# Performance work log

Hardware: AMD Instinct MI355X
Metric: run time of the kernel (lower is better)

Reference implementation:

```python
import jax, jax.numpy as jnp
import numpy as np

HEADS = 16
DIM_HEAD = 64
LN_EPS = 1e-5
COS_EPS = 1e-8


def setup_inputs() -> dict:
    key = jax.random.key(0)
    ks = jax.random.split(key, 5)
    dim = 1024
    inner = HEADS * DIM_HEAD
    q = jax.random.normal(ks[0], (4, 1024, dim), dtype=jnp.float32)
    k = jax.random.normal(ks[1], (4, 2048, dim), dtype=jnp.float32)
    v = jax.random.normal(ks[2], (4, 2048, dim), dtype=jnp.float32)
    W_in = jax.random.normal(ks[3], (dim, inner), dtype=jnp.float32) * (1.0 / np.sqrt(dim))
    W_out = jax.random.normal(ks[4], (inner, dim), dtype=jnp.float32) * (1.0 / np.sqrt(inner))
    ln_gamma = jnp.ones((dim,), dtype=jnp.float32)
    ln_beta = jnp.zeros((dim,), dtype=jnp.float32)
    b_out = jnp.zeros((dim,), dtype=jnp.float32)
    return {"q": q, "k": k, "v": v, "ln_gamma": ln_gamma, "ln_beta": ln_beta,
            "W_in": W_in, "W_out": W_out, "b_out": b_out}


def _layernorm(x, gamma, beta):
    mu = jnp.mean(x, axis=-1, keepdims=True)
    var = jnp.mean(jnp.square(x - mu), axis=-1, keepdims=True)  # biased, as torch
    return (x - mu) * jax.lax.rsqrt(var + LN_EPS) * gamma + beta


def _project(t, gamma, beta, W_in):
    # LayerNorm -> Linear(no bias) -> split heads: b n (h d) -> b h n d
    x = _layernorm(t, gamma, beta) @ W_in
    b, n, _ = x.shape
    return x.reshape(b, n, HEADS, DIM_HEAD).transpose(0, 2, 1, 3)


def reference(q, k, v, ln_gamma, ln_beta, W_in, W_out, b_out):
    f_q = _project(q, ln_gamma, ln_beta, W_in)  # [b,h,n,d]
    f_k = _project(k, ln_gamma, ln_beta, W_in)  # [b,h,m,d]
    f_v = _project(v, ln_gamma, ln_beta, W_in)  # [b,h,m,d]
    dots = jnp.einsum('bhnd,bhmd->bhnm', f_q, f_k)
    qn = jnp.linalg.norm(f_q, axis=-1, keepdims=True)          # [b,h,n,1]
    kn = jnp.linalg.norm(f_k, axis=-1, keepdims=True)          # [b,h,m,1]
    attn = dots / (qn * kn.transpose(0, 1, 3, 2) + COS_EPS)    # [b,h,n,m]
    out = jnp.einsum('bhnm,bhmd->bhnd', attn, f_v)             # [b,h,n,d]
    b, h, n, d = out.shape
    out = out.transpose(0, 2, 1, 3).reshape(b, n, h * d)       # b n (h d)
    return out @ W_out + b_out
```

## Files before the change

### kernel.cpp

```cpp
#include <hip/hip_runtime.h>

constexpr int BATCH = 4;
constexpr int SEQQ  = 1024;
constexpr int SEQK  = 2048;
constexpr int DIM   = 1024;
constexpr int NH    = 16;
constexpr int DH    = 64;
constexpr int RQ    = BATCH * SEQQ;
constexpr int RK    = BATCH * SEQK;
constexpr int RTOT  = RQ + 2 * RK;
constexpr int BH    = BATCH * NH;
constexpr int NSLC  = 8;
constexpr float LN_EPS = 1e-5f;

typedef _Float16 f16;
typedef __attribute__((ext_vector_type(8))) _Float16 f16x8;
typedef __attribute__((ext_vector_type(4))) float f32x4;

__device__ __forceinline__ void async16(const void* g, void* l) {
  __builtin_amdgcn_global_load_lds(
      (const __attribute__((address_space(1))) void*)g,
      (__attribute__((address_space(3))) void*)l, 16, 0, 0);
}

__global__ void __launch_bounds__(256) pre_kernel(
    const float* __restrict__ q, const float* __restrict__ k,
    const float* __restrict__ v, const float* __restrict__ gamma,
    const float* __restrict__ beta, f16* __restrict__ a_h,
    const float* __restrict__ W0, const float* __restrict__ W1,
    f16* __restrict__ T0, f16* __restrict__ T1) {
  __shared__ float tile[32][33];
  if (blockIdx.x < RTOT / 4) {
    const int row = blockIdx.x * 4 + (threadIdx.x >> 6);
    const int lane = threadIdx.x & 63;
    const float* src;
    if (row < RQ)            src = q + (size_t)row * DIM;
    else if (row < RQ + RK)  src = k + (size_t)(row - RQ) * DIM;
    else                     src = v + (size_t)(row - RQ - RK) * DIM;
    float4 x[4];
    float s = 0.f, s2 = 0.f;
#pragma unroll
    for (int c = 0; c < 4; c++) {
      x[c] = ((const float4*)src)[c * 64 + lane];
      s  += x[c].x + x[c].y + x[c].z + x[c].w;
      s2 += x[c].x * x[c].x + x[c].y * x[c].y + x[c].z * x[c].z + x[c].w * x[c].w;
    }
#pragma unroll
    for (int off = 1; off < 64; off <<= 1) {
      s  += __shfl_xor(s, off);
      s2 += __shfl_xor(s2, off);
    }
    const float mu = s / DIM;
    const float rs = rsqrtf(s2 / DIM - mu * mu + LN_EPS);
#pragma unroll
    for (int c = 0; c < 4; c++) {
      float4 g = ((const float4*)gamma)[c * 64 + lane];
      float4 b = ((const float4*)beta)[c * 64 + lane];
      union { f16 h[4]; uint2 u; } o;
      o.h[0] = (f16)((x[c].x - mu) * rs * g.x + b.x);
      o.h[1] = (f16)((x[c].y - mu) * rs * g.y + b.y);
      o.h[2] = (f16)((x[c].z - mu) * rs * g.z + b.z);
      o.h[3] = (f16)((x[c].w - mu) * rs * g.w + b.w);
      ((uint2*)(a_h + (size_t)row * DIM))[c * 64 + lane] = o.u;
    }
  } else {
    const int tz = blockIdx.x - RTOT / 4;
    const float* W = (tz >= 1024) ? W1 : W0;
    f16* T = (tz >= 1024) ? T1 : T0;
    const int rem = tz & 1023;
    const int k0 = (rem & 31) * 32, n0 = (rem >> 5) * 32;
    int tx = threadIdx.x & 31, ty = threadIdx.x >> 5;
#pragma unroll
    for (int i = 0; i < 4; i++)
      tile[ty + 8 * i][tx] = W[(size_t)(k0 + ty + 8 * i) * DIM + n0 + tx];
    __syncthreads();
#pragma unroll
    for (int i = 0; i < 4; i++)
      T[(size_t)(n0 + ty + 8 * i) * DIM + k0 + tx] = (f16)tile[tx][ty + 8 * i];
  }
}

constexpr int PT_A = 320 * 64;
constexpr int PT_B = 256 * 64;

#define STAGE_A(buf, kt) do {                                        \
    const f16* s_ = gA + (size_t)(kt) * 64;                          \
    f16* d_ = AsW + (buf) * PT_A;                                    \
    async16(s_,          d_);                                        \
    async16(s_ +  65536, d_ + 4096);                                 \
    async16(s_ + 131072, d_ + 8192);                                 \
    async16(s_ + 196608, d_ + 12288);                                \
    async16(s_ + 262144, d_ + 16384);                                \
  } while (0)

#define STAGE_B(buf, kt) do {                                        \
    const f16* s_ = gB + (size_t)(kt) * 64;                          \
    f16* d_ = BsW + (buf) * PT_B;                                    \
    async16(s_,          d_);                                        \
    async16(s_ +  65536, d_ + 4096);                                 \
    async16(s_ + 131072, d_ + 8192);                                 \
    async16(s_ + 196608, d_ + 12288);                                \
  } while (0)

#define STAGE_AB(buf, kt) do { STAGE_A(buf, kt); STAGE_B(buf, kt); } while (0)

#define WT0 asm volatile("s_waitcnt vmcnt(0)" ::: "memory")
#define WTN ((void)0)
#define STN ((void)0)

#define HALF(BUF, H)                                                 \
    _Pragma("unroll") for (int j_ = 0; j_ < 4; ++j_)                 \
      bf[j_] = *(const f16x8*)(bB##H + (BUF) * PT_B + j_ * 1024);    \
    _Pragma("unroll") for (int f_ = 0; f_ < 5; ++f_)                 \
      af0[f_] = *(const f16x8*)(aB##H + (BUF) * PT_A + f_ * 1024);   \
    _Pragma("unroll") for (int f_ = 0; f_ < 5; ++f_)                 \
      af1[f_] = *(const f16x8*)(aB##H + (BUF) * PT_A + 5120 +        \
                                f_ * 1024);                          \
    __builtin_amdgcn_s_setprio(1);                                   \
    _Pragma("unroll") for (int f_ = 0; f_ < 5; ++f_)                 \
      _Pragma("unroll") for (int j_ = 0; j_ < 4; ++j_)               \
        acc[f_][j_] = __builtin_amdgcn_mfma_f32_16x16x32_f16(        \
            af0[f_], bf[j_], acc[f_][j_], 0, 0, 0);                  \
    _Pragma("unroll") for (int f_ = 0; f_ < 5; ++f_)                 \
      _Pragma("unroll") for (int j_ = 0; j_ < 4; ++j_)               \
        acc[5 + f_][j_] = __builtin_amdgcn_mfma_f32_16x16x32_f16(    \
            af1[f_], bf[j_], acc[5 + f_][j_], 0, 0, 0);              \
    __builtin_amdgcn_s_setprio(0);

#define PTILE(BUF, STG, TVW) {                                       \
    __builtin_amdgcn_s_barrier();                                    \
    __builtin_amdgcn_sched_barrier(0);                               \
    STG;                                                             \
    HALF(BUF, 0)                                                     \
    HALF(BUF, 1)                                                     \
    __builtin_amdgcn_sched_barrier(0);                               \
    TVW;                                                             \
  }

__global__ void __launch_bounds__(512, 2) proj_gemm(
    const f16* __restrict__ A, const f16* __restrict__ Bt,
    f16* __restrict__ C) {
  __shared__ __align__(16) f16 As[2 * PT_A];
  __shared__ __align__(16) f16 Bs[2 * PT_B];

  const int tid = threadIdx.x;
  const int wid = tid >> 6;
  const int lane = tid & 63;
  const int la15 = lane & 15;

  const int bid = blockIdx.x;
  const int swz = (bid & 7) * 32 + (bid >> 3);
  const int row0 = (swz >> 2) * 320;
  const int col0 = (swz & 3) * 256;

  const int wm = (wid >> 2) * 160;
  const int wn = (wid & 3) * 64;

  const int hs = (tid & 7) ^ ((tid >> 3) & 7);
  const f16* gA = A + (size_t)(row0 + (tid >> 3)) * DIM + (hs >> 2) * 32 +
                  (hs & 3) * 8;
  const f16* gB = Bt + (size_t)(col0 + (tid >> 3)) * DIM + (hs >> 2) * 32 +
                  (hs & 3) * 8;
  f16* AsW = As + wid * 512;
  f16* BsW = Bs + wid * 512;

  const int g = lane >> 4;
  const int r7 = la15 & 7;
  const int cs0 = (g ^ r7) * 8;
  const int cs1 = ((4 + g) ^ r7) * 8;
  const f16* aB0 = As + (wm + la15) * 64 + cs0;
  const f16* aB1 = As + (wm + la15) * 64 + cs1;
  const f16* bB0 = Bs + (wn + la15) * 64 + cs0;
  const f16* bB1 = Bs + (wn + la15) * 64 + cs1;

  f32x4 acc[10][4];
#pragma unroll
  for (int i = 0; i < 10; i++)
#pragma unroll
    for (int j = 0; j < 4; j++) acc[i][j] = (f32x4){0.f, 0.f, 0.f, 0.f};
  f16x8 af0[5], af1[5], bf[4];

  STAGE_AB(0, 0);
  __builtin_amdgcn_sched_barrier(0);
  WT0;

#pragma unroll 1
  for (int it = 0; it < 7; ++it) {
    const int t1 = 2 * it + 1, t2 = 2 * it + 2;
    PTILE(0, STAGE_AB(1, t1), WT0)
    PTILE(1, STAGE_AB(0, t2), WT0)
  }
  PTILE(0, STAGE_AB(1, 15), WT0)
  PTILE(1, STN, WTN)

  const int crow = (lane >> 4) * 4;
#pragma unroll
  for (int mh = 0; mh < 2; ++mh)
#pragma unroll
    for (int f = 0; f < 5; ++f) {
      const int m = mh * 5 + f;
      const int rbase = row0 + wm + mh * 80 + f * 16 + crow;
#pragma unroll
      for (int r = 0; r < 4; ++r) {
        float s = acc[m][0][r] * acc[m][0][r] + acc[m][1][r] * acc[m][1][r]
                + acc[m][2][r] * acc[m][2][r] + acc[m][3][r] * acc[m][3][r];
        s += __shfl_xor(s, 1);
        s += __shfl_xor(s, 2);
        s += __shfl_xor(s, 4);
        s += __shfl_xor(s, 8);
        if (rbase + r < RQ + RK) {
          const float inv = rsqrtf(s);
#pragma unroll
          for (int j = 0; j < 4; ++j) acc[m][j][r] *= inv;
        }
      }
    }

  f16* sc = As;
  const int wmi = wid >> 2;
  const int ehalf = tid >> 8;
  const int err = (tid >> 4) & 15;
  const int ecc = tid & 15;
  const f16* rb_l = sc + ehalf * (16 * 264) + err * 264 + ecc * 16;
#pragma unroll
  for (int mh = 0; mh < 2; ++mh)
#pragma unroll
    for (int f = 0; f < 5; ++f) {
      const int m = mh * 5 + f;
#pragma unroll
      for (int j = 0; j < 4; ++j)
#pragma unroll
        for (int r = 0; r < 4; ++r)
          sc[wmi * (16 * 264) + (crow + r) * 264 + wn + j * 16 + la15] =
              (f16)acc[m][j][r];
      __syncthreads();
      f16x8 v0 = *(const f16x8*)(rb_l);
      f16x8 v1 = *(const f16x8*)(rb_l + 8);
      const int grow = row0 + ehalf * 160 + mh * 80 + f * 16 + err;
      f16* Cp = C + (size_t)grow * DIM + col0 + ecc * 16;
      *(f16x8*)(Cp) = v0;
      *(f16x8*)(Cp + 8) = v1;
      if (!(mh == 1 && f == 4)) __syncthreads();
    }
}

__global__ void __launch_bounds__(256) s_kernel(
    const f16* __restrict__ f, float* __restrict__ S4) {
  const int bh = blockIdx.x;
  const int b = bh >> 4, h = bh & 15;
  const int mbase = blockIdx.y * (SEQK / NSLC);
  const int t = threadIdx.x;
  __shared__ float ks[32][68];
  __shared__ float vs[32][68];
  const int lm   = t >> 3;
  const int lseg = (t & 7) * 8;
  const int d1 = (t & 15) * 4;
  const int d2 = (t >> 4) * 4;
  float acc[4][4] = {{0.f}};
  const f16* fk_base = f + ((size_t)RQ + (size_t)b * SEQK) * DIM + h * DH;
  const f16* fv_base = f + ((size_t)RQ + RK + (size_t)b * SEQK) * DIM + h * DH;

  int m = mbase + lm;
  f16x8 kv = *(const f16x8*)(fk_base + (size_t)m * DIM + lseg);
  f16x8 vv = *(const f16x8*)(fv_base + (size_t)m * DIM + lseg);

  constexpr int SUBS = SEQK / NSLC / 32;
  for (int sub = 0; sub < SUBS; ++sub) {
    __syncthreads();
#pragma unroll
    for (int e = 0; e < 8; e++) {
      ks[lm][lseg + e] = (float)kv[e];
      vs[lm][lseg + e] = (float)vv[e];
    }
    __syncthreads();
    if (sub + 1 < SUBS) {
      m = mbase + (sub + 1) * 32 + lm;
      kv = *(const f16x8*)(fk_base + (size_t)m * DIM + lseg);
      vv = *(const f16x8*)(fv_base + (size_t)m * DIM + lseg);
    }
#pragma unroll
    for (int mm = 0; mm < 32; ++mm) {
      float4 kk = *(const float4*)&ks[mm][d1];
      float4 vv2 = *(const float4*)&vs[mm][d2];
      acc[0][0] = fmaf(kk.x, vv2.x, acc[0][0]);
      acc[0][1] = fmaf(kk.x, vv2.y, acc[0][1]);
      acc[0][2] = fmaf(kk.x, vv2.z, acc[0][2]);
      acc[0][3] = fmaf(kk.x, vv2.w, acc[0][3]);
      acc[1][0] = fmaf(kk.y, vv2.x, acc[1][0]);
      acc[1][1] = fmaf(kk.y, vv2.y, acc[1][1]);
      acc[1][2] = fmaf(kk.y, vv2.z, acc[1][2]);
      acc[1][3] = fmaf(kk.y, vv2.w, acc[1][3]);
      acc[2][0] = fmaf(kk.z, vv2.x, acc[2][0]);
      acc[2][1] = fmaf(kk.z, vv2.y, acc[2][1]);
      acc[2][2] = fmaf(kk.z, vv2.z, acc[2][2]);
      acc[2][3] = fmaf(kk.z, vv2.w, acc[2][3]);
      acc[3][0] = fmaf(kk.w, vv2.x, acc[3][0]);
      acc[3][1] = fmaf(kk.w, vv2.y, acc[3][1]);
      acc[3][2] = fmaf(kk.w, vv2.z, acc[3][2]);
      acc[3][3] = fmaf(kk.w, vv2.w, acc[3][3]);
    }
  }
  float* Sp = S4 + ((size_t)blockIdx.y * BH + bh) * DH * DH;
#pragma unroll
  for (int i = 0; i < 4; i++)
#pragma unroll
    for (int j = 0; j < 4; j++)
      Sp[(d1 + i) * DH + (d2 + j)] = acc[i][j];
}

__global__ void __launch_bounds__(256) s_reduce(
    const float* __restrict__ S4, f16* __restrict__ Sh) {
  const int bh = blockIdx.x;
  const int t = threadIdx.x;
  const size_t base = (size_t)bh * DH * DH + t * 16;
  constexpr size_t STR = (size_t)BH * DH * DH;
#pragma unroll
  for (int c = 0; c < 4; c++) {
    float4 s = {0.f, 0.f, 0.f, 0.f};
#pragma unroll
    for (int p = 0; p < NSLC; p++) {
      float4 sp = *(const float4*)(S4 + base + p * STR + 4 * c);
      s.x += sp.x; s.y += sp.y; s.z += sp.z; s.w += sp.w;
    }
    union { f16 h[4]; uint2 u; } o;
    o.h[0] = (f16)s.x; o.h[1] = (f16)s.y; o.h[2] = (f16)s.z; o.h[3] = (f16)s.w;
    *(uint2*)(Sh + base + 4 * c) = o.u;
  }
}

__global__ void __launch_bounds__(256) m_build(
    const f16* __restrict__ wt_out, const f16* __restrict__ Sh,
    f16* __restrict__ Mt) {
  const int n0 = blockIdx.x * 128;
  const int bh = blockIdx.y;
  const int b = bh >> 4, h = bh & 15;
  __shared__ f16 Asl[128 * 64];
  __shared__ f16 Bsl[64 * 64];
  const int t = threadIdx.x;
  const int wid = t >> 6, lane = t & 63;

  const f16* gA = wt_out + (size_t)(n0 + 32 * wid + (lane >> 3)) * DIM
                  + 64 * h + (lane & 7) * 8;
  f16* lA = Asl + 32 * wid * 64;
  const f16* gB = Sh + (size_t)bh * DH * DH + (16 * wid + (lane >> 3)) * 64
                  + (lane & 7) * 8;
  f16* lB = Bsl + 16 * wid * 64;
#pragma unroll
  for (int o = 0; o < 4; o++) async16(gA + (size_t)(8 * o) * DIM, lA + 8 * o * 64);
  async16(gB, lB);
  async16(gB + 8 * 64, lB + 8 * 64);
  __syncthreads();

  const int wm = (wid >> 1) * 64;
  const int wn = (wid & 1) * 32;
  const int mrow = lane & 15;
  f32x4 acc[4][2];
#pragma unroll
  for (int i = 0; i < 4; i++)
#pragma unroll
    for (int j = 0; j < 2; j++) acc[i][j] = (f32x4){0.f, 0.f, 0.f, 0.f};

#pragma unroll
  for (int kh = 0; kh < 2; kh++) {
    const int kq = kh * 32 + (lane >> 4) * 8;
    f16x8 af[4], bf[2];
#pragma unroll
    for (int i = 0; i < 4; i++)
      af[i] = *(const f16x8*)(Asl + (wm + i * 16 + mrow) * 64 + kq);
#pragma unroll
    for (int j = 0; j < 2; j++)
      bf[j] = *(const f16x8*)(Bsl + (wn + j * 16 + mrow) * 64 + kq);
#pragma unroll
    for (int i = 0; i < 4; i++)
#pragma unroll
      for (int j = 0; j < 2; j++)
        acc[i][j] = __builtin_amdgcn_mfma_f32_16x16x32_f16(af[i], bf[j], acc[i][j], 0, 0, 0);
  }

  const int ccol = lane & 15;
  const int crow = (lane >> 4) * 4;
  f16* Mb = Mt + (size_t)b * DIM * DIM;
#pragma unroll
  for (int j = 0; j < 2; j++) {
    const int col = 64 * h + wn + j * 16 + ccol;
#pragma unroll
    for (int i = 0; i < 4; i++) {
      f16* Mp = Mb + (size_t)(n0 + wm + i * 16 + crow) * DIM + col;
#pragma unroll
      for (int r = 0; r < 4; r++) Mp[(size_t)r * DIM] = (f16)acc[i][j][r];
    }
  }
}

constexpr int FT_SZ = 128 * 64;

#define FSTG(P, gp, kt, buf) do {                                    \
    const f16* s_ = (gp) + (size_t)(kt) * 64;                        \
    f16* d_ = (P) + (buf) * FT_SZ;                                   \
    async16(s_,         d_);                                         \
    async16(s_ + 65536, d_ + 4096);                                  \
  } while (0)

#define FHALF(BUF, H)                                                \
    _Pragma("unroll") for (int j_ = 0; j_ < 2; ++j_)                 \
      gbf[j_] = *(const f16x8*)(bB##H + (BUF) * FT_SZ + j_ * 1024);  \
    _Pragma("unroll") for (int i_ = 0; i_ < 4; ++i_)                 \
      gaf[i_] = *(const f16x8*)(aB##H + (BUF) * FT_SZ + i_ * 1024);  \
    __builtin_amdgcn_s_setprio(1);                                   \
    _Pragma("unroll") for (int i_ = 0; i_ < 4; ++i_)                 \
      _Pragma("unroll") for (int j_ = 0; j_ < 2; ++j_)               \
        facc[i_][j_] = __builtin_amdgcn_mfma_f32_16x16x32_f16(       \
            gaf[i_], gbf[j_], facc[i_][j_], 0, 0, 0);                \
    __builtin_amdgcn_s_setprio(0);

#define FTILE(BUF, STG, TVW) {                                       \
    __builtin_amdgcn_s_barrier();                                    \
    __builtin_amdgcn_sched_barrier(0);                               \
    STG;                                                             \
    FHALF(BUF, 0)                                                    \
    FHALF(BUF, 1)                                                    \
    __builtin_amdgcn_sched_barrier(0);                               \
    TVW;                                                             \
  }

__global__ void __launch_bounds__(512, 2) fin_gemm(
    const f16* __restrict__ f, const f16* __restrict__ Mt,
    const float* __restrict__ bias, float* __restrict__ out) {
  __shared__ __align__(16) f16 As[2 * FT_SZ];
  __shared__ __align__(16) f16 Bs[2 * FT_SZ];
  const int tid = threadIdx.x;
  const int wid = tid >> 6;
  const int lane = tid & 63;
  const int la15 = lane & 15;

  const int bid = blockIdx.x;
  const int swz = (bid & 7) * 32 + (bid >> 3);
  const int b  = swz >> 6;
  const int rt = (swz >> 3) & 7;
  const int ct = swz & 7;
  const int grow0 = b * SEQQ + rt * 128;
  const int col0 = ct * 128;

  const int wm = (wid >> 2) * 64;
  const int wn = (wid & 3) * 32;

  const int hs = (tid & 7) ^ ((tid >> 3) & 7);
  const f16* gA = f + (size_t)(grow0 + (tid >> 3)) * DIM + (hs >> 2) * 32 +
                  (hs & 3) * 8;
  const f16* gB = Mt + (size_t)b * DIM * DIM +
                  (size_t)(col0 + (tid >> 3)) * DIM + (hs >> 2) * 32 +
                  (hs & 3) * 8;
  f16* AsW = As + wid * 512;
  f16* BsW = Bs + wid * 512;

  const int g = lane >> 4;
  const int r7 = la15 & 7;
  const int cs0 = (g ^ r7) * 8;
  const int cs1 = ((4 + g) ^ r7) * 8;
  const f16* aB0 = As + (wm + la15) * 64 + cs0;
  const f16* aB1 = As + (wm + la15) * 64 + cs1;
  const f16* bB0 = Bs + (wn + la15) * 64 + cs0;
  const f16* bB1 = Bs + (wn + la15) * 64 + cs1;

  f32x4 facc[4][2];
#pragma unroll
  for (int i = 0; i < 4; i++)
#pragma unroll
    for (int j = 0; j < 2; j++) facc[i][j] = (f32x4){0.f, 0.f, 0.f, 0.f};
  f16x8 gaf[4], gbf[2];

  FSTG(AsW, gA, 0, 0);
  FSTG(BsW, gB, 0, 0);
  __builtin_amdgcn_sched_barrier(0);
  WT0;

#pragma unroll 1
  for (int it = 0; it < 7; ++it) {
    const int t1 = 2 * it + 1, t2 = 2 * it + 2;
    FTILE(0, { FSTG(AsW, gA, t1, 1); FSTG(BsW, gB, t1, 1); }, WT0)
    FTILE(1, { FSTG(AsW, gA, t2, 0); FSTG(BsW, gB, t2, 0); }, WT0)
  }
  FTILE(0, { FSTG(AsW, gA, 15, 1); FSTG(BsW, gB, 15, 1); }, WT0)
  FTILE(1, STN, WTN)

  const int crow = (lane >> 4) * 4;
#pragma unroll
  for (int j = 0; j < 2; ++j) {
    const int col = col0 + wn + j * 16 + la15;
    const float bv = bias[col];
#pragma unroll
    for (int i = 0; i < 4; ++i) {
      float* Op = out + (size_t)(grow0 + wm + i * 16 + crow) * DIM + col;
#pragma unroll
      for (int r = 0; r < 4; ++r) Op[(size_t)r * DIM] = facc[i][j][r] + bv;
    }
  }
}

extern "C" void kernel_launch(void* const* d_in, const int* in_sizes, int n_in,
                              void* d_out, int out_size, void* d_ws, size_t ws_size,
                              hipStream_t stream) {
  const float* q     = (const float*)d_in[0];
  const float* k     = (const float*)d_in[1];
  const float* v     = (const float*)d_in[2];
  const float* gamma = (const float*)d_in[3];
  const float* beta  = (const float*)d_in[4];
  const float* W_in  = (const float*)d_in[5];
  const float* W_out = (const float*)d_in[6];
  const float* b_out = (const float*)d_in[7];
  float* out = (float*)d_out;

  char* w = (char*)d_ws;
  f16*   f      = (f16*)w;
  f16*   a_h    = f + (size_t)RTOT * DIM;
  f16*   wt_in  = a_h + (size_t)RTOT * DIM;
  f16*   wt_out = wt_in + (size_t)DIM * DIM;
  f16*   Mt     = wt_out + (size_t)DIM * DIM;
  f16*   Sh     = Mt + (size_t)BATCH * DIM * DIM;
  float* S4     = (float*)(Sh + (size_t)BH * DH * DH);

  pre_kernel<<<RTOT / 4 + 2048, 256, 0, stream>>>(
      q, k, v, gamma, beta, a_h, W_in, W_out, wt_in, wt_out);

  proj_gemm<<<dim3(256), 512, 0, stream>>>(a_h, wt_in, f);

  s_kernel<<<dim3(BH, NSLC), 256, 0, stream>>>(f, S4);

  s_reduce<<<BH, 256, 0, stream>>>(S4, Sh);

  m_build<<<dim3(DIM / 128, BH), 256, 0, stream>>>(wt_out, Sh, Mt);

  fin_gemm<<<dim3(256), 512, 0, stream>>>(f, Mt, b_out, out);
}
```

Baseline: 229.0 us.

## Apply per-head S to Q before W_out instead of building per-batch M

The old path folded each head's S matrix into W_out to build a per-batch 1024x1024 matrix M, then ran the final GEMM against M. The new path adds an attn_kernel that reduces the S partial slices in LDS and multiplies the normalized query features by S per head, writing a per-row attention output. The final GEMM then uses the shared W_out for all batches. This removes the s_reduce and m_build launches and the large per-batch M write and read, at the cost of a new small per-head GEMM kernel and a transposed S store.

```diff
diff --git a/kernel.cpp b/kernel.cpp
--- a/kernel.cpp
+++ b/kernel.cpp
@@ -302,92 +302,92 @@
   }
   float* Sp = S4 + ((size_t)blockIdx.y * BH + bh) * DH * DH;
 #pragma unroll
-  for (int i = 0; i < 4; i++)
-#pragma unroll
-    for (int j = 0; j < 4; j++)
-      Sp[(d1 + i) * DH + (d2 + j)] = acc[i][j];
-}
-
-__global__ void __launch_bounds__(256) s_reduce(
-    const float* __restrict__ S4, f16* __restrict__ Sh) {
-  const int bh = blockIdx.x;
-  const int t = threadIdx.x;
-  const size_t base = (size_t)bh * DH * DH + t * 16;
-  constexpr size_t STR = (size_t)BH * DH * DH;
-#pragma unroll
-  for (int c = 0; c < 4; c++) {
-    float4 s = {0.f, 0.f, 0.f, 0.f};
-#pragma unroll
-    for (int p = 0; p < NSLC; p++) {
-      float4 sp = *(const float4*)(S4 + base + p * STR + 4 * c);
-      s.x += sp.x; s.y += sp.y; s.z += sp.z; s.w += sp.w;
-    }
-    union { f16 h[4]; uint2 u; } o;
-    o.h[0] = (f16)s.x; o.h[1] = (f16)s.y; o.h[2] = (f16)s.z; o.h[3] = (f16)s.w;
-    *(uint2*)(Sh + base + 4 * c) = o.u;
-  }
-}
-
-__global__ void __launch_bounds__(256) m_build(
-    const f16* __restrict__ wt_out, const f16* __restrict__ Sh,
-    f16* __restrict__ Mt) {
-  const int n0 = blockIdx.x * 128;
+  for (int j = 0; j < 4; j++)
+#pragma unroll
+    for (int i = 0; i < 4; i++)
+      Sp[(d2 + j) * DH + (d1 + i)] = acc[i][j];
+}
+
+__global__ void __launch_bounds__(256) attn_kernel(
+    const f16* __restrict__ f, const float* __restrict__ S4,
+    f16* __restrict__ ao) {
+  const int rt = blockIdx.x;
   const int bh = blockIdx.y;
   const int b = bh >> 4, h = bh & 15;
-  __shared__ f16 Asl[128 * 64];
-  __shared__ f16 Bsl[64 * 64];
-  const int t = threadIdx.x;
-  const int wid = t >> 6, lane = t & 63;
-
-  const f16* gA = wt_out + (size_t)(n0 + 32 * wid + (lane >> 3)) * DIM
-                  + 64 * h + (lane & 7) * 8;
-  f16* lA = Asl + 32 * wid * 64;
-  const f16* gB = Sh + (size_t)bh * DH * DH + (16 * wid + (lane >> 3)) * 64
-                  + (lane & 7) * 8;
-  f16* lB = Bsl + 16 * wid * 64;
-#pragma unroll
-  for (int o = 0; o < 4; o++) async16(gA + (size_t)(8 * o) * DIM, lA + 8 * o * 64);
-  async16(gB, lB);
-  async16(gB + 8 * 64, lB + 8 * 64);
+  const int grow0 = b * SEQQ + rt * 128;
+  __shared__ __align__(16) f16 Al[128 * 64];
+  __shared__ __align__(16) f16 Bl[64 * 72];
+  const int tid = threadIdx.x;
+  const int wid = tid >> 6;
+  const int lane = tid & 63;
+  const int la15 = lane & 15;
+
+  const int hsA = (lane & 7) ^ ((lane >> 3) & 7);
+  const f16* gq = f + (size_t)(grow0 + wid * 32 + (lane >> 3)) * DIM +
+                  h * DH + (hsA >> 2) * 32 + (hsA & 3) * 8;
+  f16* lA = Al + wid * 32 * 64;
+#pragma unroll
+  for (int o = 0; o < 4; o++)
+    async16(gq + (size_t)(8 * o) * DIM, lA + 8 * o * 64);
+
+  const float* Sp = S4 + (size_t)bh * DH * DH + tid * 16;
+  constexpr size_t STR = (size_t)BH * DH * DH;
+  float4 sv[4];
+#pragma unroll
+  for (int c = 0; c < 4; c++) sv[c] = (float4){0.f, 0.f, 0.f, 0.f};
+#pragma unroll
+  for (int p = 0; p < NSLC; p++)
+#pragma unroll
+    for (int c = 0; c < 4; c++) {
+      float4 x = *(const float4*)(Sp + p * STR + 4 * c);
+      sv[c].x += x.x; sv[c].y += x.y; sv[c].z += x.z; sv[c].w += x.w;
+    }
+  f16* bw = Bl + (tid >> 2) * 72 + (tid & 3) * 16;
+#pragma unroll
+  for (int c = 0; c < 4; c++) {
+    union { f16 h4[4]; uint2 u; } o;
+    o.h4[0] = (f16)sv[c].x; o.h4[1] = (f16)sv[c].y;
+    o.h4[2] = (f16)sv[c].z; o.h4[3] = (f16)sv[c].w;
+    *(uint2*)(bw + 4 * c) = o.u;
+  }
+  WT0;
   __syncthreads();
 
-  const int wm = (wid >> 1) * 64;
-  const int wn = (wid & 1) * 32;
-  const int mrow = lane & 15;
-  f32x4 acc[4][2];
-#pragma unroll
-  for (int i = 0; i < 4; i++)
-#pragma unroll
-    for (int j = 0; j < 2; j++) acc[i][j] = (f32x4){0.f, 0.f, 0.f, 0.f};
-
-#pragma unroll
-  for (int kh = 0; kh < 2; kh++) {
-    const int kq = kh * 32 + (lane >> 4) * 8;
-    f16x8 af[4], bf[2];
-#pragma unroll
-    for (int i = 0; i < 4; i++)
-      af[i] = *(const f16x8*)(Asl + (wm + i * 16 + mrow) * 64 + kq);
-#pragma unroll
-    for (int j = 0; j < 2; j++)
-      bf[j] = *(const f16x8*)(Bsl + (wn + j * 16 + mrow) * 64 + kq);
-#pragma unroll
-    for (int i = 0; i < 4; i++)
-#pragma unroll
-      for (int j = 0; j < 2; j++)
-        acc[i][j] = __builtin_amdgcn_mfma_f32_16x16x32_f16(af[i], bf[j], acc[i][j], 0, 0, 0);
-  }
-
-  const int ccol = lane & 15;
+  const int g2 = lane >> 4;
+  f32x4 acc[2][4];
+#pragma unroll
+  for (int i = 0; i < 2; i++)
+#pragma unroll
+    for (int j = 0; j < 4; j++) acc[i][j] = (f32x4){0.f, 0.f, 0.f, 0.f};
+#pragma unroll
+  for (int ks = 0; ks < 2; ks++) {
+    f16x8 af[2], bf[4];
+#pragma unroll
+    for (int i = 0; i < 2; i++) {
+      const int row = wid * 32 + i * 16 + la15;
+      const int cs = ((ks * 4 + g2) ^ (row & 7)) * 8;
+      af[i] = *(const f16x8*)(Al + row * 64 + cs);
+    }
+#pragma unroll
+    for (int j = 0; j < 4; j++)
+      bf[j] = *(const f16x8*)(Bl + (j * 16 + la15) * 72 + ks * 32 + g2 * 8);
+#pragma unroll
+    for (int i = 0; i < 2; i++)
+#pragma unroll
+      for (int j = 0; j < 4; j++)
+        acc[i][j] = __builtin_amdgcn_mfma_f32_16x16x32_f16(
+            af[i], bf[j], acc[i][j], 0, 0, 0);
+  }
+
   const int crow = (lane >> 4) * 4;
-  f16* Mb = Mt + (size_t)b * DIM * DIM;
-#pragma unroll
-  for (int j = 0; j < 2; j++) {
-    const int col = 64 * h + wn + j * 16 + ccol;
-#pragma unroll
-    for (int i = 0; i < 4; i++) {
-      f16* Mp = Mb + (size_t)(n0 + wm + i * 16 + crow) * DIM + col;
-#pragma unroll
-      for (int r = 0; r < 4; r++) Mp[(size_t)r * DIM] = (f16)acc[i][j][r];
+#pragma unroll
+  for (int j = 0; j < 4; j++) {
+    const int col = h * DH + j * 16 + la15;
+#pragma unroll
+    for (int i = 0; i < 2; i++) {
+      f16* op = ao + (size_t)(grow0 + wid * 32 + i * 16 + crow) * DIM + col;
+#pragma unroll
+      for (int r = 0; r < 4; r++) op[(size_t)r * DIM] = (f16)acc[i][j][r];
     }
   }
 }
@@ -424,7 +424,7 @@
   }
 
 __global__ void __launch_bounds__(512, 2) fin_gemm(
-    const f16* __restrict__ f, const f16* __restrict__ Mt,
+    const f16* __restrict__ ao, const f16* __restrict__ Bt,
     const float* __restrict__ bias, float* __restrict__ out) {
   __shared__ __align__(16) f16 As[2 * FT_SZ];
   __shared__ __align__(16) f16 Bs[2 * FT_SZ];
@@ -435,20 +435,18 @@
 
   const int bid = blockIdx.x;
   const int swz = (bid & 7) * 32 + (bid >> 3);
-  const int b  = swz >> 6;
-  const int rt = (swz >> 3) & 7;
+  const int rt = swz >> 3;
   const int ct = swz & 7;
-  const int grow0 = b * SEQQ + rt * 128;
+  const int grow0 = rt * 128;
   const int col0 = ct * 128;
 
   const int wm = (wid >> 2) * 64;
   const int wn = (wid & 3) * 32;
 
   const int hs = (tid & 7) ^ ((tid >> 3) & 7);
-  const f16* gA = f + (size_t)(grow0 + (tid >> 3)) * DIM + (hs >> 2) * 32 +
+  const f16* gA = ao + (size_t)(grow0 + (tid >> 3)) * DIM + (hs >> 2) * 32 +
                   (hs & 3) * 8;
-  const f16* gB = Mt + (size_t)b * DIM * DIM +
-                  (size_t)(col0 + (tid >> 3)) * DIM + (hs >> 2) * 32 +
+  const f16* gB = Bt + (size_t)(col0 + (tid >> 3)) * DIM + (hs >> 2) * 32 +
                   (hs & 3) * 8;
   f16* AsW = As + wid * 512;
   f16* BsW = Bs + wid * 512;
@@ -515,8 +513,8 @@
   f16*   a_h    = f + (size_t)RTOT * DIM;
   f16*   wt_in  = a_h + (size_t)RTOT * DIM;
   f16*   wt_out = wt_in + (size_t)DIM * DIM;
-  f16*   Mt     = wt_out + (size_t)DIM * DIM;
-  f16*   Sh     = Mt + (size_t)BATCH * DIM * DIM;
+  f16*   ao     = wt_out + (size_t)DIM * DIM;
+  f16*   Sh     = ao + (size_t)BATCH * DIM * DIM;
   float* S4     = (float*)(Sh + (size_t)BH * DH * DH);
 
   pre_kernel<<<RTOT / 4 + 2048, 256, 0, stream>>>(
@@ -526,9 +524,7 @@
 
   s_kernel<<<dim3(BH, NSLC), 256, 0, stream>>>(f, S4);
 
-  s_reduce<<<BH, 256, 0, stream>>>(S4, Sh);
-
-  m_build<<<dim3(DIM / 128, BH), 256, 0, stream>>>(wt_out, Sh, Mt);
-
-  fin_gemm<<<dim3(256), 512, 0, stream>>>(f, Mt, b_out, out);
-}
+  attn_kernel<<<dim3(8, BH), 256, 0, stream>>>(f, S4, ao);
+
+  fin_gemm<<<dim3(256), 512, 0, stream>>>(ao, wt_out, b_out, out);
+}
```

Result: slower. 244.6 us (+6.8%).
